# Kernel optimization log

Hardware: AMD Instinct MI355X
Metric: run time of the kernel (lower is better)

Reference implementation:

```python
import jax, jax.numpy as jnp
import numpy as np

N_NODES, N_EDGES = 50000, 800000
IN_DIM, HID, HEADS, OUT_DIM = 768, 64, 4, 256
B, A = 128, 4
SLOPE = 0.2  # args.alpha (LeakyReLU negative slope)


def _p(key, shape, scale=0.02):
    return scale * jax.random.normal(key, shape, dtype=jnp.float32)


def setup_inputs() -> dict:
    key = jax.random.key(0)
    ks = jax.random.split(key, 32)
    inp = {
        "x": jax.random.normal(ks[0], (N_NODES, IN_DIM), dtype=jnp.float32),
        "pooled": jax.random.normal(ks[1], (B, IN_DIM), dtype=jnp.float32),
        "src": jax.random.randint(ks[2], (N_EDGES,), 0, N_NODES, dtype=jnp.int32),
        "dst": jax.random.randint(ks[3], (N_EDGES,), 0, N_NODES, dtype=jnp.int32),
        "aspect_idx": jax.random.randint(ks[4], (B, A), 0, N_NODES, dtype=jnp.int32),
    }
    # GATv2 layer dims: (in, out_per_head, heads)
    dims = [(IN_DIM, HID, HEADS), (HID * HEADS, HID, HEADS), (HID * HEADS, OUT_DIM, 1)]
    k = 5
    for i, (fi, fo, h) in enumerate(dims):
        inp[f"Ws{i}"] = _p(ks[k], (fi, h * fo)); k += 1
        inp[f"bs{i}"] = jnp.zeros((h * fo,), jnp.float32)
        inp[f"Wd{i}"] = _p(ks[k], (fi, h * fo)); k += 1
        inp[f"bd{i}"] = jnp.zeros((h * fo,), jnp.float32)
        inp[f"attn{i}"] = _p(ks[k], (h, fo)); k += 1
    inp["Wc1"] = _p(ks[k], (OUT_DIM + IN_DIM, OUT_DIM)); k += 1
    inp["bc1"] = jnp.zeros((OUT_DIM,), jnp.float32)
    inp["Wc2"] = _p(ks[k], (OUT_DIM, OUT_DIM)); k += 1
    inp["bc2"] = jnp.zeros((OUT_DIM,), jnp.float32)
    inp["Wc3"] = _p(ks[k], (OUT_DIM, OUT_DIM)); k += 1
    inp["bc3"] = jnp.zeros((OUT_DIM,), jnp.float32)
    return inp


def gatv2_layer(x, src, dst, Ws, bs, Wd, bd, attn, heads, fout):
    """DGL GATv2Conv (eval mode, allow_zero_in_degree=True)."""
    n = x.shape[0]
    fs = (x @ Ws + bs).reshape(n, heads, fout)   # fc_src
    fd = (x @ Wd + bd).reshape(n, heads, fout)   # fc_dst
    e = jax.nn.leaky_relu(fs[src] + fd[dst], SLOPE)        # [E,H,F]
    scores = jnp.einsum('ehf,hf->eh', e, attn)             # [E,H]
    # edge softmax over incoming edges of each dst node
    m = jax.ops.segment_max(scores, dst, num_segments=n)
    ex = jnp.exp(scores - m[dst])
    denom = jax.ops.segment_sum(ex, dst, num_segments=n)
    alpha = ex / denom[dst]
    # aggregate messages: out[v] = sum_{(u->v)} alpha * fs[u]  -> [N,H,F]
    return jax.ops.segment_sum(alpha[:, :, None] * fs[src], dst, num_segments=n)


def reference(x, pooled, src, dst, aspect_idx,
              Ws0, bs0, Wd0, bd0, attn0,
              Ws1, bs1, Wd1, bd1, attn1,
              Ws2, bs2, Wd2, bd2, attn2,
              Wc1, bc1, Wc2, bc2, Wc3, bc3):
    n = x.shape[0]
    h = gatv2_layer(x, src, dst, Ws0, bs0, Wd0, bd0, attn0, HEADS, HID).reshape(n, -1)
    h = gatv2_layer(h, src, dst, Ws1, bs1, Wd1, bd1, attn1, HEADS, HID).reshape(n, -1)
    h = gatv2_layer(h, src, dst, Ws2, bs2, Wd2, bd2, attn2, 1, OUT_DIM)[:, 0, :]  # squeeze(1)
    aspect_feats = jnp.mean(h[aspect_idx], axis=1)          # [B, OUT_DIM]
    combined = jnp.concatenate([aspect_feats, pooled], axis=1)
    z = combined @ Wc1 + bc1
    z = z @ Wc2 + bc2
    z = jax.nn.relu(z)
    return z @ Wc3 + bc3                                    # [B, OUT_DIM]
```

## Files before the change

kernel.cpp:

```cpp
#include <hip/hip_runtime.h>
#include <hip/hip_bf16.h>
#include <math.h>

#define SLOPE 0.2f

typedef unsigned short u16;
typedef __attribute__((ext_vector_type(8))) short short8;
typedef __attribute__((ext_vector_type(4))) float f32x4;

__device__ __forceinline__ u16 f2bf(float x) {
    __hip_bfloat16 h = __float2bfloat16(x);
    return *reinterpret_cast<u16*>(&h);
}
__device__ __forceinline__ float bf2f(u16 h) {
    union { unsigned u; float f; } c; c.u = ((unsigned)h) << 16; return c.f;
}

__device__ __forceinline__ void gload16(const u16* g, u16* lds) {
    __builtin_amdgcn_global_load_lds(
        (__attribute__((address_space(1))) void*)const_cast<u16*>(g),
        (__attribute__((address_space(3))) void*)lds, 16, 0, 0);
}

__global__ __launch_bounds__(256) void k_zero_int(int* __restrict__ p, int n) {
    int i = blockIdx.x * 256 + threadIdx.x;
    if (i < n) p[i] = 0;
}

__global__ __launch_bounds__(256) void k_count(const int* __restrict__ dst,
                                               int* __restrict__ cnt, int E) {
    int e = blockIdx.x * 256 + threadIdx.x;
    if (e < E) atomicAdd(&cnt[dst[e]], 1);
}

__global__ __launch_bounds__(1024) void k_scan(const int* __restrict__ cnt,
                                               int* __restrict__ off, int n) {
    __shared__ int part[1024];
    int t = threadIdx.x;
    int chunk = (n + 1023) / 1024;
    int base = t * chunk;
    int s = 0;
    for (int i = 0; i < chunk; i++) {
        int idx = base + i;
        if (idx < n) s += cnt[idx];
    }
    part[t] = s;
    __syncthreads();
    for (int o = 1; o < 1024; o <<= 1) {
        int v = (t >= o) ? part[t - o] : 0;
        __syncthreads();
        part[t] += v;
        __syncthreads();
    }
    int run = (t == 0) ? 0 : part[t - 1];
    for (int i = 0; i < chunk; i++) {
        int idx = base + i;
        if (idx < n) { off[idx] = run; run += cnt[idx]; }
    }
    if (t == 1023) off[n] = part[1023];
}

__global__ __launch_bounds__(256) void k_scatter(const int* __restrict__ dst,
                                                 const int* __restrict__ src,
                                                 const int* __restrict__ off,
                                                 int* __restrict__ cur,
                                                 int* __restrict__ srcs, int E) {
    int e = blockIdx.x * 256 + threadIdx.x;
    if (e >= E) return;
    int d = dst[e];
    int pos = atomicAdd(&cur[d], 1);
    srcs[off[d] + pos] = src[e];
}

__global__ __launch_bounds__(256) void k_f2bf(const float* __restrict__ src,
                                              u16* __restrict__ dst,
                                              int n_valid, int n_pad) {
    int i4 = (blockIdx.x * 256 + threadIdx.x) * 4;
    if (i4 >= n_pad) return;
    u16 o0 = 0, o1 = 0, o2 = 0, o3 = 0;
    if (i4 < n_valid) {
        float4 v = *(const float4*)(src + i4);
        o0 = f2bf(v.x); o1 = f2bf(v.y); o2 = f2bf(v.z); o3 = f2bf(v.w);
    }
    ushort4 o; o.x = o0; o.y = o1; o.z = o2; o.w = o3;
    *(ushort4*)(dst + i4) = o;
}

__global__ __launch_bounds__(256) void k_wT6(
    const float* __restrict__ W0, const float* __restrict__ W1,
    const float* __restrict__ W2, const float* __restrict__ W3,
    const float* __restrict__ W4, const float* __restrict__ W5,
    u16* __restrict__ T0, u16* __restrict__ T1, u16* __restrict__ T2,
    u16* __restrict__ T3, u16* __restrict__ T4, u16* __restrict__ T5) {
    int z = blockIdx.z;
    const float* W; u16* T; int K;
    switch (z) {
        case 0: W = W0; T = T0; K = 768; break;
        case 1: W = W1; T = T1; K = 768; break;
        case 2: W = W2; T = T2; K = 256; break;
        case 3: W = W3; T = T3; K = 256; break;
        case 4: W = W4; T = T4; K = 256; break;
        default: W = W5; T = T5; K = 256; break;
    }
    int idx = blockIdx.x * 256 + threadIdx.x;
    if (idx >= K * 256) return;
    int k = idx >> 8, c = idx & 255;
    T[c * K + k] = f2bf(W[idx]);
}

__global__ __launch_bounds__(256) void k_gemm_bf16(
    const u16* __restrict__ A, int K, int N,
    const u16* __restrict__ BTs, const u16* __restrict__ BTd,
    const float* __restrict__ bias_s, const float* __restrict__ bias_d,
    u16* __restrict__ Cs, u16* __restrict__ Cd) {
    __shared__ u16 Ash[128 * 32];
    __shared__ u16 Bsh[128 * 32];
    const u16* BT = blockIdx.z ? BTd : BTs;
    const float* bias = blockIdx.z ? bias_d : bias_s;
    u16* C = blockIdx.z ? Cd : Cs;
    int by128 = blockIdx.y * 128;
    int c0 = blockIdx.x * 128;
    int t = threadIdx.x;
    int w = t >> 6, l = t & 63;
    int wr = w >> 1, wc = w & 1;
    int lr = l & 15, lk = l >> 4;

    f32x4 acc[4][4];
#pragma unroll
    for (int m = 0; m < 4; m++)
#pragma unroll
        for (int n = 0; n < 4; n++) acc[m][n] = (f32x4){0.f, 0.f, 0.f, 0.f};

    int srow = w * 32 + (l >> 2);
    int skq = (l & 3) * 8;

    for (int k0 = 0; k0 < K; k0 += 32) {
#pragma unroll
        for (int j = 0; j < 2; j++) {
            const u16* ga = A + (size_t)(by128 + srow + j * 16) * K + k0 + skq;
            gload16(ga, Ash + w * 1024 + j * 512);
            const u16* gb = BT + (size_t)(c0 + srow + j * 16) * K + k0 + skq;
            gload16(gb, Bsh + w * 1024 + j * 512);
        }
        __syncthreads();
        short8 af[4], bfr[4];
#pragma unroll
        for (int m = 0; m < 4; m++)
            af[m] = *(const short8*)&Ash[(wr * 64 + m * 16 + lr) * 32 + lk * 8];
#pragma unroll
        for (int n = 0; n < 4; n++)
            bfr[n] = *(const short8*)&Bsh[(wc * 64 + n * 16 + lr) * 32 + lk * 8];
#pragma unroll
        for (int m = 0; m < 4; m++)
#pragma unroll
            for (int n = 0; n < 4; n++)
                acc[m][n] = __builtin_amdgcn_mfma_f32_16x16x32_bf16(af[m], bfr[n], acc[m][n], 0, 0, 0);
        __syncthreads();
    }

#pragma unroll
    for (int n = 0; n < 4; n++) {
        int gcol = c0 + wc * 64 + n * 16 + lr;
        float bv = bias[gcol];
#pragma unroll
        for (int m = 0; m < 4; m++) {
#pragma unroll
            for (int j = 0; j < 4; j++) {
                int grow = by128 + wr * 64 + m * 16 + lk * 4 + j;
                if (grow < N) C[(size_t)grow * 256 + gcol] = f2bf(acc[m][n][j] + bv);
            }
        }
    }
}

template <int G, int OUTBF>
__global__ __launch_bounds__(256) void k_gat_aggregate(
    const u16* __restrict__ fs, const u16* __restrict__ fd,
    const float* __restrict__ attn,
    const int* __restrict__ off, const int* __restrict__ srcs,
    void* __restrict__ outv, int n, int npad) {
    int v = blockIdx.x * 4 + (threadIdx.x >> 6);
    if (v >= npad) return;
    int lane = threadIdx.x & 63;
    size_t base = (size_t)v * 256 + lane * 4;
    int e0 = 0, e1 = 0;
    if (v < n) { e0 = off[v]; e1 = off[v + 1]; }
    if (e0 == e1) {
        if (OUTBF) {
            ushort4 z; z.x = z.y = z.z = z.w = 0;
            *(ushort4*)((u16*)outv + base) = z;
        } else {
            *(float4*)((float*)outv + base) = make_float4(0.f, 0.f, 0.f, 0.f);
        }
        return;
    }
    float4 wat = *(const float4*)(attn + lane * 4);
    ushort4 fdq = *(const ushort4*)(fd + base);
    float fdx = bf2f(fdq.x), fdy = bf2f(fdq.y), fdz = bf2f(fdq.z), fdw = bf2f(fdq.w);

    float denom = 0.f;
    float ax = 0.f, ay = 0.f, az = 0.f, aw = 0.f;

    int s0 = srcs[e0];
    ushort4 fq = *(const ushort4*)(fs + (size_t)s0 * 256 + lane * 4);
    for (int i = e0; i < e1; i++) {
        int inx = (i + 1 < e1) ? (i + 1) : i;
        int sn = srcs[inx];
        ushort4 fqn = *(const ushort4*)(fs + (size_t)sn * 256 + lane * 4);

        float fx = bf2f(fq.x), fy = bf2f(fq.y), fz = bf2f(fq.z), fw = bf2f(fq.w);
        float ex = fx + fdx, ey = fy + fdy, ez = fz + fdz, ew = fw + fdw;
        ex = fmaxf(ex, SLOPE * ex);
        ey = fmaxf(ey, SLOPE * ey);
        ez = fmaxf(ez, SLOPE * ez);
        ew = fmaxf(ew, SLOPE * ew);
        float p = ex * wat.x + ey * wat.y + ez * wat.z + ew * wat.w;
#pragma unroll
        for (int m = 1; m < G; m <<= 1) p += __shfl_xor(p, m, 64);
        float wgt = __expf(p);
        denom += wgt;
        ax = fmaf(wgt, fx, ax);
        ay = fmaf(wgt, fy, ay);
        az = fmaf(wgt, fz, az);
        aw = fmaf(wgt, fw, aw);
        fq = fqn;
    }
    float inv = 1.f / denom;
    if (OUTBF) {
        ushort4 o;
        o.x = f2bf(ax * inv); o.y = f2bf(ay * inv);
        o.z = f2bf(az * inv); o.w = f2bf(aw * inv);
        *(ushort4*)((u16*)outv + base) = o;
    } else {
        *(float4*)((float*)outv + base) = make_float4(ax * inv, ay * inv, az * inv, aw * inv);
    }
}

__global__ __launch_bounds__(256) void k_head(
    const float* __restrict__ h, const int* __restrict__ aidx,
    const float* __restrict__ pooled,
    const float* __restrict__ Wc1, const float* __restrict__ bc1,
    const float* __restrict__ Wc2, const float* __restrict__ bc2,
    const float* __restrict__ Wc3, const float* __restrict__ bc3,
    float* __restrict__ out) {
    __shared__ float comb[1024];
    __shared__ float z[256];
    int b = blockIdx.x, t = threadIdx.x;
    float s = 0.f;
#pragma unroll
    for (int j = 0; j < 4; j++) {
        int node = aidx[b * 4 + j];
        s += h[(size_t)node * 256 + t];
    }
    comb[t] = s * 0.25f;
    for (int k = t; k < 768; k += 256) comb[256 + k] = pooled[(size_t)b * 768 + k];
    __syncthreads();
    float a1 = bc1[t];
    for (int k = 0; k < 1024; k++) a1 = fmaf(comb[k], Wc1[(size_t)k * 256 + t], a1);
    __syncthreads();
    z[t] = a1;
    __syncthreads();
    float a2 = bc2[t];
    for (int k = 0; k < 256; k++) a2 = fmaf(z[k], Wc2[(size_t)k * 256 + t], a2);
    a2 = fmaxf(a2, 0.f);
    __syncthreads();
    z[t] = a2;
    __syncthreads();
    float a3 = bc3[t];
    for (int k = 0; k < 256; k++) a3 = fmaf(z[k], Wc3[(size_t)k * 256 + t], a3);
    out[(size_t)b * 256 + t] = a3;
}

extern "C" void kernel_launch(void* const* d_in, const int* in_sizes, int n_in,
                              void* d_out, int out_size, void* d_ws, size_t ws_size,
                              hipStream_t stream) {
    const float* x = (const float*)d_in[0];
    const float* pooled = (const float*)d_in[1];
    const int* src = (const int*)d_in[2];
    const int* dst = (const int*)d_in[3];
    const int* aidx = (const int*)d_in[4];
    const float* Ws0 = (const float*)d_in[5];
    const float* bs0 = (const float*)d_in[6];
    const float* Wd0 = (const float*)d_in[7];
    const float* bd0 = (const float*)d_in[8];
    const float* attn0 = (const float*)d_in[9];
    const float* Ws1 = (const float*)d_in[10];
    const float* bs1 = (const float*)d_in[11];
    const float* Wd1 = (const float*)d_in[12];
    const float* bd1 = (const float*)d_in[13];
    const float* attn1 = (const float*)d_in[14];
    const float* Ws2 = (const float*)d_in[15];
    const float* bs2 = (const float*)d_in[16];
    const float* Wd2 = (const float*)d_in[17];
    const float* bd2 = (const float*)d_in[18];
    const float* attn2 = (const float*)d_in[19];
    const float* Wc1 = (const float*)d_in[20];
    const float* bc1 = (const float*)d_in[21];
    const float* Wc2 = (const float*)d_in[22];
    const float* bc2 = (const float*)d_in[23];
    const float* Wc3 = (const float*)d_in[24];
    const float* bc3 = (const float*)d_in[25];

    const int N = in_sizes[0] / 768;
    const int E = in_sizes[2];
    const int NT = (N + 127) / 128;
    const int NPAD = NT * 128;

    char* ws = (char*)d_ws;
    size_t o = 0;
    auto carve = [&](size_t bytes) {
        char* p = ws + o;
        o = (o + bytes + 255) & ~(size_t)255;
        return p;
    };
    u16* fs_bf = (u16*)carve((size_t)NPAD * 256 * 2);
    u16* fd_bf = (u16*)carve((size_t)NPAD * 256 * 2);
    char* bigbuf = carve((size_t)NPAD * 768 * 2);
    int* cnt = (int*)carve((size_t)2 * N * 4);
    int* cur = cnt + N;
    int* off = (int*)carve((size_t)(N + 1) * 4);
    int* srcs = (int*)carve((size_t)E * 4);
    u16* WT0s = (u16*)carve((size_t)256 * 768 * 2);
    u16* WT0d = (u16*)carve((size_t)256 * 768 * 2);
    u16* WT1s = (u16*)carve((size_t)256 * 256 * 2);
    u16* WT1d = (u16*)carve((size_t)256 * 256 * 2);
    u16* WT2s = (u16*)carve((size_t)256 * 256 * 2);
    u16* WT2d = (u16*)carve((size_t)256 * 256 * 2);
    (void)ws_size;

    u16* Xbf = (u16*)bigbuf;
    float* h3 = (float*)bigbuf;
    u16* Hbf = (u16*)const_cast<float*>(x);

    const int aggblocks = (NPAD + 3) / 4;
    const dim3 gemm_grid(2, NT, 2);

    k_zero_int<<<(2 * N + 255) / 256, 256, 0, stream>>>(cnt, 2 * N);
    k_count<<<(E + 255) / 256, 256, 0, stream>>>(dst, cnt, E);
    k_scan<<<1, 1024, 0, stream>>>(cnt, off, N);
    k_scatter<<<(E + 255) / 256, 256, 0, stream>>>(dst, src, off, cur, srcs, E);

    k_wT6<<<dim3(768, 1, 6), 256, 0, stream>>>(Ws0, Wd0, Ws1, Wd1, Ws2, Wd2,
                                               WT0s, WT0d, WT1s, WT1d, WT2s, WT2d);

    k_f2bf<<<((NPAD * 768 / 4) + 255) / 256, 256, 0, stream>>>(x, Xbf, N * 768, NPAD * 768);
    k_gemm_bf16<<<gemm_grid, 256, 0, stream>>>(Xbf, 768, N, WT0s, WT0d, bs0, bd0, fs_bf, fd_bf);
    k_gat_aggregate<16, 1><<<aggblocks, 256, 0, stream>>>(fs_bf, fd_bf, attn0, off, srcs, Hbf, N, NPAD);

    k_gemm_bf16<<<gemm_grid, 256, 0, stream>>>(Hbf, 256, N, WT1s, WT1d, bs1, bd1, fs_bf, fd_bf);
    k_gat_aggregate<16, 1><<<aggblocks, 256, 0, stream>>>(fs_bf, fd_bf, attn1, off, srcs, Hbf, N, NPAD);

    k_gemm_bf16<<<gemm_grid, 256, 0, stream>>>(Hbf, 256, N, WT2s, WT2d, bs2, bd2, fs_bf, fd_bf);
    k_gat_aggregate<64, 0><<<(N + 3) / 4, 256, 0, stream>>>(fs_bf, fd_bf, attn2, off, srcs, h3, N, N);

    k_head<<<128, 256, 0, stream>>>(h3, aidx, pooled, Wc1, bc1, Wc2, bc2, Wc3, bc3, (float*)d_out);
}
```

Baseline: 979.3 us.

## Fuse fp32-to-bf16 conversion into GEMM, concatenate src/dst weights, XCD-aware tiling

Removes the separate x-to-bf16 conversion pass by converting fp32 rows on the fly inside the first GEMM's A-tile load. The src and dst weights are concatenated into one 512-wide transposed matrix, so each GEMM is a single 1D launch. That launch remaps block ids so neighbouring tiles land on the same XCD and share the A tile in cache. The epilogue now stages the output through LDS and writes coalesced 16-byte rows instead of scattered 2-byte stores. The trade-off is that layer 0 loads A through registers instead of async global-to-LDS copies, and it uses dedicated buffers instead of aliasing the input.

```diff
diff --git a/kernel.cpp b/kernel.cpp
--- a/kernel.cpp
+++ b/kernel.cpp
@@ -72,54 +72,45 @@
     srcs[off[d] + pos] = src[e];
 }
 
-__global__ __launch_bounds__(256) void k_f2bf(const float* __restrict__ src,
-                                              u16* __restrict__ dst,
-                                              int n_valid, int n_pad) {
-    int i4 = (blockIdx.x * 256 + threadIdx.x) * 4;
-    if (i4 >= n_pad) return;
-    u16 o0 = 0, o1 = 0, o2 = 0, o3 = 0;
-    if (i4 < n_valid) {
-        float4 v = *(const float4*)(src + i4);
-        o0 = f2bf(v.x); o1 = f2bf(v.y); o2 = f2bf(v.z); o3 = f2bf(v.w);
-    }
-    ushort4 o; o.x = o0; o.y = o1; o.z = o2; o.w = o3;
-    *(ushort4*)(dst + i4) = o;
-}
-
-__global__ __launch_bounds__(256) void k_wT6(
-    const float* __restrict__ W0, const float* __restrict__ W1,
-    const float* __restrict__ W2, const float* __restrict__ W3,
-    const float* __restrict__ W4, const float* __restrict__ W5,
+__global__ __launch_bounds__(256) void k_wcat(
+    const float* __restrict__ Ws0, const float* __restrict__ Wd0,
+    const float* __restrict__ bs0, const float* __restrict__ bd0,
+    const float* __restrict__ Ws1, const float* __restrict__ Wd1,
+    const float* __restrict__ bs1, const float* __restrict__ bd1,
+    const float* __restrict__ Ws2, const float* __restrict__ Wd2,
+    const float* __restrict__ bs2, const float* __restrict__ bd2,
     u16* __restrict__ T0, u16* __restrict__ T1, u16* __restrict__ T2,
-    u16* __restrict__ T3, u16* __restrict__ T4, u16* __restrict__ T5) {
+    float* __restrict__ bc0, float* __restrict__ bc1, float* __restrict__ bc2) {
     int z = blockIdx.z;
-    const float* W; u16* T; int K;
-    switch (z) {
-        case 0: W = W0; T = T0; K = 768; break;
-        case 1: W = W1; T = T1; K = 768; break;
-        case 2: W = W2; T = T2; K = 256; break;
-        case 3: W = W3; T = T3; K = 256; break;
-        case 4: W = W4; T = T4; K = 256; break;
-        default: W = W5; T = T5; K = 256; break;
-    }
+    const float *Ws, *Wd, *bs, *bd; u16* T; float* bc; int K;
+    if (z == 0)      { Ws = Ws0; Wd = Wd0; bs = bs0; bd = bd0; T = T0; bc = bc0; K = 768; }
+    else if (z == 1) { Ws = Ws1; Wd = Wd1; bs = bs1; bd = bd1; T = T1; bc = bc1; K = 256; }
+    else             { Ws = Ws2; Wd = Wd2; bs = bs2; bd = bd2; T = T2; bc = bc2; K = 256; }
     int idx = blockIdx.x * 256 + threadIdx.x;
+    if (blockIdx.x == 0) { bc[idx] = bs[idx]; bc[idx + 256] = bd[idx]; }
     if (idx >= K * 256) return;
     int k = idx >> 8, c = idx & 255;
-    T[c * K + k] = f2bf(W[idx]);
-}
-
-__global__ __launch_bounds__(256) void k_gemm_bf16(
-    const u16* __restrict__ A, int K, int N,
-    const u16* __restrict__ BTs, const u16* __restrict__ BTd,
-    const float* __restrict__ bias_s, const float* __restrict__ bias_d,
+    T[(size_t)c * K + k] = f2bf(Ws[idx]);
+    T[(size_t)(c + 256) * K + k] = f2bf(Wd[idx]);
+}
+
+template <int AF32>
+__global__ __launch_bounds__(256) void k_gemm2(
+    const void* __restrict__ Av, int K, int N,
+    const u16* __restrict__ BT, const float* __restrict__ bcat,
     u16* __restrict__ Cs, u16* __restrict__ Cd) {
-    __shared__ u16 Ash[128 * 32];
-    __shared__ u16 Bsh[128 * 32];
-    const u16* BT = blockIdx.z ? BTd : BTs;
-    const float* bias = blockIdx.z ? bias_d : bias_s;
-    u16* C = blockIdx.z ? Cd : Cs;
-    int by128 = blockIdx.y * 128;
-    int c0 = blockIdx.x * 128;
+    __shared__ u16 smem[128 * 136];
+    u16* Ash = smem;
+    u16* Bsh = smem + 4096;
+
+    int nblk = gridDim.x;
+    int bid = blockIdx.x;
+    int q = nblk >> 3, r = nblk & 7;
+    int xcd = bid & 7, rank = bid >> 3;
+    int lgc = (xcd < r ? xcd * (q + 1) : r * (q + 1) + (xcd - r) * q) + rank;
+    int row0 = (lgc >> 2) * 128;
+    int c0 = (lgc & 3) * 128;
+
     int t = threadIdx.x;
     int w = t >> 6, l = t & 63;
     int wr = w >> 1, wc = w & 1;
@@ -135,10 +126,32 @@
     int skq = (l & 3) * 8;
 
     for (int k0 = 0; k0 < K; k0 += 32) {
+        if (AF32) {
+            const float* Af = (const float*)Av;
+#pragma unroll
+            for (int j = 0; j < 2; j++) {
+                int grow = row0 + srow + j * 16;
+                int gr = grow < N ? grow : N - 1;
+                const float* ga = Af + (size_t)gr * K + k0 + skq;
+                float4 v0 = *(const float4*)ga;
+                float4 v1 = *(const float4*)(ga + 4);
+                short8 pk;
+                pk[0] = (short)f2bf(v0.x); pk[1] = (short)f2bf(v0.y);
+                pk[2] = (short)f2bf(v0.z); pk[3] = (short)f2bf(v0.w);
+                pk[4] = (short)f2bf(v1.x); pk[5] = (short)f2bf(v1.y);
+                pk[6] = (short)f2bf(v1.z); pk[7] = (short)f2bf(v1.w);
+                *(short8*)&Ash[w * 1024 + j * 512 + l * 8] = pk;
+            }
+        } else {
+            const u16* Ab = (const u16*)Av;
+#pragma unroll
+            for (int j = 0; j < 2; j++) {
+                const u16* ga = Ab + (size_t)(row0 + srow + j * 16) * K + k0 + skq;
+                gload16(ga, Ash + w * 1024 + j * 512);
+            }
+        }
 #pragma unroll
         for (int j = 0; j < 2; j++) {
-            const u16* ga = A + (size_t)(by128 + srow + j * 16) * K + k0 + skq;
-            gload16(ga, Ash + w * 1024 + j * 512);
             const u16* gb = BT + (size_t)(c0 + srow + j * 16) * K + k0 + skq;
             gload16(gb, Bsh + w * 1024 + j * 512);
         }
@@ -160,16 +173,27 @@
 
 #pragma unroll
     for (int n = 0; n < 4; n++) {
-        int gcol = c0 + wc * 64 + n * 16 + lr;
-        float bv = bias[gcol];
-#pragma unroll
-        for (int m = 0; m < 4; m++) {
+        int ecol = wc * 64 + n * 16 + lr;
+        float bv = bcat[c0 + ecol];
+#pragma unroll
+        for (int m = 0; m < 4; m++)
 #pragma unroll
             for (int j = 0; j < 4; j++) {
-                int grow = by128 + wr * 64 + m * 16 + lk * 4 + j;
-                if (grow < N) C[(size_t)grow * 256 + gcol] = f2bf(acc[m][n][j] + bv);
+                int erow = wr * 64 + m * 16 + lk * 4 + j;
+                smem[erow * 136 + ecol] = f2bf(acc[m][n][j] + bv);
             }
-        }
+    }
+    __syncthreads();
+    int er = t >> 1, half = t & 1;
+    int grow = row0 + er;
+    if (grow < N) {
+        int gc = c0 + half * 64;
+        u16* Crow = (gc < 256) ? (Cs + (size_t)grow * 256 + gc)
+                               : (Cd + (size_t)grow * 256 + gc - 256);
+        const u16* sp = &smem[er * 136 + half * 64];
+#pragma unroll
+        for (int i = 0; i < 8; i++)
+            *(short8*)(Crow + i * 8) = *(const short8*)(sp + i * 8);
     }
 }
 
@@ -315,42 +339,39 @@
     };
     u16* fs_bf = (u16*)carve((size_t)NPAD * 256 * 2);
     u16* fd_bf = (u16*)carve((size_t)NPAD * 256 * 2);
-    char* bigbuf = carve((size_t)NPAD * 768 * 2);
+    u16* Hbf   = (u16*)carve((size_t)NPAD * 256 * 2);
+    float* h3  = (float*)carve((size_t)N * 256 * 4);
     int* cnt = (int*)carve((size_t)2 * N * 4);
     int* cur = cnt + N;
     int* off = (int*)carve((size_t)(N + 1) * 4);
     int* srcs = (int*)carve((size_t)E * 4);
-    u16* WT0s = (u16*)carve((size_t)256 * 768 * 2);
-    u16* WT0d = (u16*)carve((size_t)256 * 768 * 2);
-    u16* WT1s = (u16*)carve((size_t)256 * 256 * 2);
-    u16* WT1d = (u16*)carve((size_t)256 * 256 * 2);
-    u16* WT2s = (u16*)carve((size_t)256 * 256 * 2);
-    u16* WT2d = (u16*)carve((size_t)256 * 256 * 2);
+    u16* WTc0 = (u16*)carve((size_t)512 * 768 * 2);
+    u16* WTc1 = (u16*)carve((size_t)512 * 256 * 2);
+    u16* WTc2 = (u16*)carve((size_t)512 * 256 * 2);
+    float* bcat0 = (float*)carve(512 * 4);
+    float* bcat1 = (float*)carve(512 * 4);
+    float* bcat2 = (float*)carve(512 * 4);
     (void)ws_size;
 
-    u16* Xbf = (u16*)bigbuf;
-    float* h3 = (float*)bigbuf;
-    u16* Hbf = (u16*)const_cast<float*>(x);
-
     const int aggblocks = (NPAD + 3) / 4;
-    const dim3 gemm_grid(2, NT, 2);
+    const int gemm_blocks = 4 * NT;
 
     k_zero_int<<<(2 * N + 255) / 256, 256, 0, stream>>>(cnt, 2 * N);
     k_count<<<(E + 255) / 256, 256, 0, stream>>>(dst, cnt, E);
     k_scan<<<1, 1024, 0, stream>>>(cnt, off, N);
     k_scatter<<<(E + 255) / 256, 256, 0, stream>>>(dst, src, off, cur, srcs, E);
 
-    k_wT6<<<dim3(768, 1, 6), 256, 0, stream>>>(Ws0, Wd0, Ws1, Wd1, Ws2, Wd2,
-                                               WT0s, WT0d, WT1s, WT1d, WT2s, WT2d);
-
-    k_f2bf<<<((NPAD * 768 / 4) + 255) / 256, 256, 0, stream>>>(x, Xbf, N * 768, NPAD * 768);
-    k_gemm_bf16<<<gemm_grid, 256, 0, stream>>>(Xbf, 768, N, WT0s, WT0d, bs0, bd0, fs_bf, fd_bf);
+    k_wcat<<<dim3(768, 1, 3), 256, 0, stream>>>(Ws0, Wd0, bs0, bd0, Ws1, Wd1, bs1, bd1,
+                                                Ws2, Wd2, bs2, bd2,
+                                                WTc0, WTc1, WTc2, bcat0, bcat1, bcat2);
+
+    k_gemm2<1><<<gemm_blocks, 256, 0, stream>>>(x, 768, N, WTc0, bcat0, fs_bf, fd_bf);
     k_gat_aggregate<16, 1><<<aggblocks, 256, 0, stream>>>(fs_bf, fd_bf, attn0, off, srcs, Hbf, N, NPAD);
 
-    k_gemm_bf16<<<gemm_grid, 256, 0, stream>>>(Hbf, 256, N, WT1s, WT1d, bs1, bd1, fs_bf, fd_bf);
+    k_gemm2<0><<<gemm_blocks, 256, 0, stream>>>(Hbf, 256, N, WTc1, bcat1, fs_bf, fd_bf);
     k_gat_aggregate<16, 1><<<aggblocks, 256, 0, stream>>>(fs_bf, fd_bf, attn1, off, srcs, Hbf, N, NPAD);
 
-    k_gemm_bf16<<<gemm_grid, 256, 0, stream>>>(Hbf, 256, N, WT2s, WT2d, bs2, bd2, fs_bf, fd_bf);
+    k_gemm2<0><<<gemm_blocks, 256, 0, stream>>>(Hbf, 256, N, WTc2, bcat2, fs_bf, fd_bf);
     k_gat_aggregate<64, 0><<<(N + 3) / 4, 256, 0, stream>>>(fs_bf, fd_bf, attn2, off, srcs, h3, N, N);
 
     k_head<<<128, 256, 0, stream>>>(h3, aidx, pooled, Wc1, bc1, Wc2, bc2, Wc3, bc3, (float*)d_out);
```

Measured after the change: 922.2 us. 5.8% less time.
